# Kernel optimization log

Hardware: AMD Instinct MI355X
Metric: run time of the kernel (lower is better)

Reference implementation:

```python
import jax, jax.numpy as jnp
import numpy as np


def _attention(v, W, static_hidden, dec_hidden):
    # static_hidden: [B,N,H], dec_hidden: [B,1,H], v: [1,1,H], W: [1,H,2H]
    hidden = jnp.concatenate(
        [static_hidden, jnp.broadcast_to(dec_hidden, static_hidden.shape)], axis=2
    )  # [B,N,2H]
    e = jnp.tanh(jnp.einsum('bnk,hk->bnh', hidden, W[0]))  # W @ hidden^T, done row-wise
    scores = jnp.einsum('bnh,h->bn', e, v[0, 0])  # [B,N]
    return jax.nn.softmax(scores, axis=1)[:, None, :]  # [B,1,N]


def _gru_step(x, h, w_ih, w_hh, b_ih, b_hh):
    # x: [B,H] input, h: [B,H] prev hidden; PyTorch gate order: r | z | n
    gx = x @ w_ih.T + b_ih  # [B,3H]
    gh = h @ w_hh.T + b_hh  # [B,3H]
    H = h.shape[-1]
    r = jax.nn.sigmoid(gx[:, :H] + gh[:, :H])
    z = jax.nn.sigmoid(gx[:, H:2 * H] + gh[:, H:2 * H])
    n = jnp.tanh(gx[:, 2 * H:] + r * gh[:, 2 * H:])
    return (1.0 - z) * n + z * h


def _pointer_scores(v, W, static_hidden, context, state_embedding):
    # energy = cat(static, context, state_emb) -> [B,N,3H]
    energy = jnp.concatenate(
        [static_hidden,
         jnp.broadcast_to(context, static_hidden.shape),
         jnp.broadcast_to(state_embedding, static_hidden.shape)], axis=2)
    e = jnp.tanh(jnp.einsum('bnk,hk->bnh', energy, W[0]))  # [B,N,H]
    return jnp.einsum('bnh,h->bn', e, v[0, 0])  # [B,N]


def setup_inputs() -> dict:
    key = jax.random.key(0)
    B, N, H = 128, 512, 512
    ks = jax.random.split(key, 16)
    s = 0.05
    return {
        'static_hidden': jax.random.normal(ks[0], (B, N, H), jnp.float32),
        'state_embedding': jax.random.normal(ks[1], (B, 1, H), jnp.float32),
        'decoder_hidden': jax.random.normal(ks[2], (B, 1, H), jnp.float32),
        'target_hidden': jax.random.normal(ks[3], (B, 1, H), jnp.float32),
        'last_hh': jax.random.normal(ks[4], (1, B, H), jnp.float32),
        # Pointer params (note: target branch of the original reuses self.v/self.W)
        'ptr_v': jax.random.normal(ks[5], (1, 1, H), jnp.float32) * s,
        'ptr_W': jax.random.normal(ks[6], (1, H, 3 * H), jnp.float32) * s,
        # encoder attention params
        'enc_v': jax.random.normal(ks[7], (1, 1, H), jnp.float32) * s,
        'enc_W': jax.random.normal(ks[8], (1, H, 2 * H), jnp.float32) * s,
        # target attention params
        'tgt_v': jax.random.normal(ks[9], (1, 1, H), jnp.float32) * s,
        'tgt_W': jax.random.normal(ks[10], (1, H, 2 * H), jnp.float32) * s,
        # GRU (single layer) params
        'gru_w_ih': jax.random.normal(ks[11], (3 * H, H), jnp.float32) * s,
        'gru_w_hh': jax.random.normal(ks[12], (3 * H, H), jnp.float32) * s,
        'gru_b_ih': jax.random.normal(ks[13], (3 * H,), jnp.float32) * s,
        'gru_b_hh': jax.random.normal(ks[14], (3 * H,), jnp.float32) * s,
    }


def reference(static_hidden, state_embedding, decoder_hidden, target_hidden, last_hh,
              ptr_v, ptr_W, enc_v, enc_W, tgt_v, tgt_W,
              gru_w_ih, gru_w_hh, gru_b_ih, gru_b_hh):
    # GRU over seq len 1 (batch_first); dropout layers are identity (eval mode)
    h_new = _gru_step(decoder_hidden[:, 0, :], last_hh[0], gru_w_ih, gru_w_hh, gru_b_ih, gru_b_hh)
    rnn_out = h_new[:, None, :]          # [B,1,H]
    new_last_hh = h_new[None]            # [1,B,H]

    # encoder attention + context
    enc_attn = _attention(enc_v, enc_W, static_hidden, rnn_out)   # [B,1,N]
    context = jnp.matmul(enc_attn, static_hidden)                 # [B,1,H]
    probs = _pointer_scores(ptr_v, ptr_W, static_hidden, context, state_embedding)

    # target attention + context (original reuses self.v/self.W for scoring)
    tgt_attn = _attention(tgt_v, tgt_W, static_hidden, target_hidden)
    context_t = jnp.matmul(tgt_attn, static_hidden)
    probs_target = _pointer_scores(ptr_v, ptr_W, static_hidden, context_t, state_embedding)

    probs = 5.0 * probs + probs_target
    return (probs, new_last_hh)
```

## Files before the change

### kernel.cpp

```cpp
#include <hip/hip_runtime.h>
#include <math.h>

#define B 128
#define N 512
#define H 512

typedef __attribute__((ext_vector_type(8))) short short8;
typedef __attribute__((ext_vector_type(4))) float floatx4;

typedef const __attribute__((address_space(1))) unsigned int* gas_t;
typedef __attribute__((address_space(3))) unsigned int* las_t;

__device__ __forceinline__ void gl16(const void* g, void* l){
    __builtin_amdgcn_global_load_lds((gas_t)g, (las_t)l, 16, 0, 0);
}

__device__ __forceinline__ float sigmoidf_(float x){ return 1.0f/(1.0f+__expf(-x)); }

__device__ __forceinline__ float fast_tanh(float x){
    float t = __expf(-2.0f*fabsf(x));
    float r = __fdividef(1.0f - t, 1.0f + t);
    return copysignf(r, x);
}

__device__ __forceinline__ unsigned f2bf1(float f){
    unsigned u = __float_as_uint(f);
    u += 0x7FFFu + ((u>>16)&1u);
    return u>>16;
}
__device__ __forceinline__ unsigned pk2(float a, float b){
    return f2bf1(a) | (f2bf1(b)<<16);
}

__global__ __launch_bounds__(256) void k_cast_small(
    const float* __restrict__ encW, const float* __restrict__ tgtW,
    const float* __restrict__ ptrW, const float* __restrict__ wih,
    const float* __restrict__ whh,
    const float* __restrict__ dec, const float* __restrict__ lhh,
    const float* __restrict__ tgt, const float* __restrict__ sem,
    unsigned short* __restrict__ We_s, unsigned short* __restrict__ Wt_s,
    unsigned short* __restrict__ Wp_s, unsigned short* __restrict__ We_d,
    unsigned short* __restrict__ Wt_d, unsigned short* __restrict__ Wp_c,
    unsigned short* __restrict__ Wp_e, unsigned short* __restrict__ Wih_b,
    unsigned short* __restrict__ Whh_b,
    unsigned short* __restrict__ Xbf, unsigned short* __restrict__ Hbf,
    unsigned short* __restrict__ Tbf, unsigned short* __restrict__ Sbf)
{
    int r = blockIdx.x, t = threadIdx.x;
    if (r < 6656){
        const float* src; unsigned short* dst; int pitch, off, row;
        if (r < 512)      { src=encW; dst=We_s; pitch=2*H; off=0;   row=r; }
        else if (r<1024)  { src=tgtW; dst=Wt_s; pitch=2*H; off=0;   row=r-512; }
        else if (r<1536)  { src=ptrW; dst=Wp_s; pitch=3*H; off=0;   row=r-1024; }
        else if (r<2048)  { src=encW; dst=We_d; pitch=2*H; off=H;   row=r-1536; }
        else if (r<2560)  { src=tgtW; dst=Wt_d; pitch=2*H; off=H;   row=r-2048; }
        else if (r<3072)  { src=ptrW; dst=Wp_c; pitch=3*H; off=H;   row=r-2560; }
        else if (r<3584)  { src=ptrW; dst=Wp_e; pitch=3*H; off=2*H; row=r-3072; }
        else if (r<5120)  { src=wih;  dst=Wih_b;pitch=H;   off=0;   row=r-3584; }
        else              { src=whh;  dst=Whh_b;pitch=H;   off=0;   row=r-5120; }
        float2 v = *(const float2*)&src[(size_t)row*pitch + off + 2*t];
        *(unsigned*)&dst[(size_t)row*H + 2*t] = pk2(v.x, v.y);
    } else {
        int blk = r - 6656; int mat = blk >> 5;
        const float* src = mat==0?dec : mat==1?lhh : mat==2?tgt : sem;
        unsigned short* dst = mat==0?Xbf : mat==1?Hbf : mat==2?Tbf : Sbf;
        size_t i = ((size_t)(blk&31)*256 + t)*8;
        float4 lo = *(const float4*)&src[i];
        float4 hi = *(const float4*)&src[i+4];
        uint4 p;
        p.x = pk2(lo.x,lo.y); p.y = pk2(lo.z,lo.w);
        p.z = pk2(hi.x,hi.y); p.w = pk2(hi.z,hi.w);
        *(uint4*)&dst[i] = p;
    }
}

__device__ __forceinline__ void gemm128_tile(
    const unsigned short* __restrict__ Ab,
    const unsigned short* __restrict__ Bb,
    float* __restrict__ C, int ldc)
{
    __shared__ __align__(16) unsigned short As[128*64];
    __shared__ __align__(16) unsigned short Bs[128*64];
    int t = threadIdx.x;
    int lane = t & 63, wave = t >> 6;
    int wy = wave >> 1, wx = wave & 1;
    int li = lane & 15, quad = lane >> 4;

    floatx4 acc[4][4];
    #pragma unroll
    for (int i=0;i<4;++i)
      #pragma unroll
      for (int j=0;j<4;++j) acc[i][j] = (floatx4)(0.0f);

    for (int kt=0; kt<8; ++kt){
        int k0 = kt*64;
        #pragma unroll
        for (int c=0;c<4;++c){
            int s = c*256 + t;
            int row = s >> 3;
            int kb = (s & 7) ^ (row & 7);
            gl16(&Ab[(size_t)row*512 + k0 + kb*8], &As[(size_t)s*8]);
            gl16(&Bb[(size_t)row*512 + k0 + kb*8], &Bs[(size_t)s*8]);
        }
        __syncthreads();
        #pragma unroll
        for (int ks=0;ks<2;++ks){
            short8 af[4], bg[4];
            #pragma unroll
            for (int i=0;i<4;++i){
                int m = wy*64 + i*16 + li;
                int kb = (ks*4 + quad) ^ (m&7);
                af[i] = *(const short8*)&As[m*64 + kb*8];
            }
            #pragma unroll
            for (int j=0;j<4;++j){
                int h = wx*64 + j*16 + li;
                int kb = (ks*4 + quad) ^ (h&7);
                bg[j] = *(const short8*)&Bs[h*64 + kb*8];
            }
            #pragma unroll
            for (int i=0;i<4;++i)
              #pragma unroll
              for (int j=0;j<4;++j)
                acc[i][j] = __builtin_amdgcn_mfma_f32_16x16x32_bf16(af[i], bg[j], acc[i][j], 0,0,0);
        }
        __syncthreads();
    }
    #pragma unroll
    for (int i=0;i<4;++i)
      #pragma unroll
      for (int j=0;j<4;++j)
        #pragma unroll
        for (int rg=0;rg<4;++rg){
            int m = wy*64 + i*16 + quad*4 + rg;
            int n = wx*64 + j*16 + li;
            C[(size_t)m*ldc + n] = acc[i][j][rg];
        }
}

__device__ __forceinline__ void gemm128_tile_f32A(
    const float* __restrict__ Af,
    const unsigned short* __restrict__ Bb,
    float* __restrict__ C, int ldc)
{
    __shared__ __align__(16) unsigned short As[128*64];
    __shared__ __align__(16) unsigned short Bs[128*64];
    int t = threadIdx.x;
    int lane = t & 63, wave = t >> 6;
    int wy = wave >> 1, wx = wave & 1;
    int li = lane & 15, quad = lane >> 4;

    floatx4 acc[4][4];
    #pragma unroll
    for (int i=0;i<4;++i)
      #pragma unroll
      for (int j=0;j<4;++j) acc[i][j] = (floatx4)(0.0f);

    for (int kt=0; kt<8; ++kt){
        int k0 = kt*64;
        #pragma unroll
        for (int c=0;c<4;++c){
            int s = c*256 + t;
            int row = s >> 3;
            int kb = (s & 7) ^ (row & 7);
            gl16(&Bb[(size_t)row*512 + k0 + kb*8], &Bs[(size_t)s*8]);
            const float* src = Af + (size_t)row*512 + k0 + kb*8;
            float4 lo = *(const float4*)src;
            float4 hi = *(const float4*)(src+4);
            uint4 p;
            p.x = pk2(lo.x,lo.y); p.y = pk2(lo.z,lo.w);
            p.z = pk2(hi.x,hi.y); p.w = pk2(hi.z,hi.w);
            *(uint4*)&As[(size_t)s*8] = p;
        }
        __syncthreads();
        #pragma unroll
        for (int ks=0;ks<2;++ks){
            short8 af[4], bg[4];
            #pragma unroll
            for (int i=0;i<4;++i){
                int m = wy*64 + i*16 + li;
                int kb = (ks*4 + quad) ^ (m&7);
                af[i] = *(const short8*)&As[m*64 + kb*8];
            }
            #pragma unroll
            for (int j=0;j<4;++j){
                int h = wx*64 + j*16 + li;
                int kb = (ks*4 + quad) ^ (h&7);
                bg[j] = *(const short8*)&Bs[h*64 + kb*8];
            }
            #pragma unroll
            for (int i=0;i<4;++i)
              #pragma unroll
              for (int j=0;j<4;++j)
                acc[i][j] = __builtin_amdgcn_mfma_f32_16x16x32_bf16(af[i], bg[j], acc[i][j], 0,0,0);
        }
        __syncthreads();
    }
    #pragma unroll
    for (int i=0;i<4;++i)
      #pragma unroll
      for (int j=0;j<4;++j)
        #pragma unroll
        for (int rg=0;rg<4;++rg){
            int m = wy*64 + i*16 + quad*4 + rg;
            int n = wx*64 + j*16 + li;
            C[(size_t)m*ldc + n] = acc[i][j][rg];
        }
}

__global__ __launch_bounds__(256,2) void k_mega(
    const unsigned short* __restrict__ Xbf, const unsigned short* __restrict__ Hbf,
    const unsigned short* __restrict__ Wih_b, const unsigned short* __restrict__ Whh_b,
    float* __restrict__ gx, float* __restrict__ gh,
    const unsigned short* __restrict__ Tbf, const unsigned short* __restrict__ Sbf,
    const unsigned short* __restrict__ Wt_d, const unsigned short* __restrict__ Wp_e,
    float* __restrict__ d_tgt, float* __restrict__ d_se,
    const float* __restrict__ A, unsigned short* __restrict__ Abf)
{
    int blk = blockIdx.x;
    if (blk < 32){
        const unsigned short *Ab, *Bb; float* C; int ldc;
        if (blk < 24){
            int mat = blk / 12, nt = blk % 12;
            Ab = mat ? Hbf : Xbf;
            Bb = (mat ? Whh_b : Wih_b) + (size_t)nt*128*512;
            C = (mat ? gh : gx) + nt*128;
            ldc = 3*H;
        } else {
            int sub = blk - 24; int mat = sub >> 2, nt = sub & 3;
            Ab = mat==0 ? Tbf : Sbf;
            Bb = (mat==0 ? Wt_d : Wp_e) + (size_t)nt*128*512;
            C = (mat==0 ? d_tgt : d_se) + nt*128;
            ldc = H;
        }
        gemm128_tile(Ab, Bb, C, ldc);
    } else {
        int t = threadIdx.x;
        size_t i = ((size_t)(blk-32)*256 + t)*8;
        float4 lo = *(const float4*)&A[i];
        float4 hi = *(const float4*)&A[i+4];
        uint4 p;
        p.x = pk2(lo.x,lo.y); p.y = pk2(lo.z,lo.w);
        p.z = pk2(hi.x,hi.y); p.w = pk2(hi.z,hi.w);
        *(uint4*)&Abf[i] = p;
    }
}

__global__ __launch_bounds__(256) void k_gru_gate(const float* __restrict__ gx,
    const float* __restrict__ gh, const float* __restrict__ lhh,
    const float* __restrict__ bih, const float* __restrict__ bhh,
    float* __restrict__ out_hh, unsigned short* __restrict__ hnew_bf)
{
    int idx = blockIdx.x*256 + threadIdx.x;
    int b = idx >> 9, k = idx & 511;
    const float* gxb = gx + (size_t)b*(3*H);
    const float* ghb = gh + (size_t)b*(3*H);
    float r = sigmoidf_(gxb[k]     + bih[k]     + ghb[k]     + bhh[k]);
    float z = sigmoidf_(gxb[H+k]   + bih[H+k]   + ghb[H+k]   + bhh[H+k]);
    float n = tanhf(gxb[2*H+k] + bih[2*H+k] + r*(ghb[2*H+k] + bhh[2*H+k]));
    float h = (1.f-z)*n + z*lhh[idx];
    out_hh[idx] = h;
    hnew_bf[idx] = (unsigned short)f2bf1(h);
}

__global__ __launch_bounds__(256,2) void k_bias_enc(
    const unsigned short* __restrict__ HNbf, const unsigned short* __restrict__ We_d,
    float* __restrict__ d_enc)
{
    int nt = blockIdx.x;
    gemm128_tile(HNbf, We_d + (size_t)nt*128*512, d_enc + nt*128, H);
}

__global__ __launch_bounds__(256,2) void k_dptr_gemm(
    const float* __restrict__ ctx, const float* __restrict__ ctxt,
    const unsigned short* __restrict__ Wp_c,
    float* __restrict__ d_pe, float* __restrict__ d_pt)
{
    int blk = blockIdx.x;
    int mat = blk >> 2, nt = blk & 3;
    const float* Af = mat ? ctxt : ctx;
    const unsigned short* Bb = Wp_c + (size_t)nt*128*512;
    float* C = (mat ? d_pt : d_pe) + nt*128;
    gemm128_tile_f32A(Af, Bb, C, H);
}

template<bool BF16A>
__global__ __launch_bounds__(256,2) void k_scores_fused(
    const float* __restrict__ Af, const unsigned short* __restrict__ Abf,
    const unsigned short* __restrict__ We, const unsigned short* __restrict__ Wt,
    const float* __restrict__ d_enc, const float* __restrict__ d_tgt,
    const float* __restrict__ enc_v, const float* __restrict__ tgt_v,
    float* __restrict__ sc_e, float* __restrict__ sc_t)
{
    __shared__ __align__(16) unsigned short As[128*64];
    __shared__ __align__(16) unsigned short Be[128*64];
    __shared__ __align__(16) unsigned short Bt[128*64];
    __shared__ float red_e[2][128], red_t[2][128];
    int blk = blockIdx.x;
    int b = blk >> 2; int nt = blk & 3;
    int n0 = nt*128;
    int t = threadIdx.x;
    int lane = t & 63, wave = t >> 6;
    int wy = wave >> 1, wx = wave & 1;
    int li = lane & 15, quad = lane >> 4;

    float nse[4][4], nst[4][4];
    #pragma unroll
    for (int i=0;i<4;++i)
      #pragma unroll
      for (int rg=0;rg<4;++rg){ nse[i][rg]=0.f; nst[i][rg]=0.f; }

    for (int ht=0; ht<4; ++ht){
        int hb = ht*128;
        floatx4 acc_e[4][4], acc_t[4][4];
        #pragma unroll
        for (int i=0;i<4;++i)
          #pragma unroll
          for (int j=0;j<4;++j){ acc_e[i][j]=(floatx4)(0.0f); acc_t[i][j]=(floatx4)(0.0f); }

        for (int kt=0; kt<8; ++kt){
            int k0 = kt*64;
            #pragma unroll
            for (int c=0;c<4;++c){
                int s = c*256 + t;
                int row = s >> 3;
                int kb = (s & 7) ^ (row & 7);
                if constexpr (BF16A){
                    gl16(&Abf[(size_t)(b*N+n0+row)*H + k0 + kb*8], &As[(size_t)s*8]);
                } else {
                    const float* src = Af + (size_t)(b*N+n0+row)*H + k0 + kb*8;
                    float4 lo = *(const float4*)src;
                    float4 hi = *(const float4*)(src+4);
                    uint4 p;
                    p.x = pk2(lo.x,lo.y); p.y = pk2(lo.z,lo.w);
                    p.z = pk2(hi.x,hi.y); p.w = pk2(hi.z,hi.w);
                    *(uint4*)&As[(size_t)s*8] = p;
                }
                gl16(&We[(size_t)(hb+row)*H + k0 + kb*8], &Be[(size_t)s*8]);
                gl16(&Wt[(size_t)(hb+row)*H + k0 + kb*8], &Bt[(size_t)s*8]);
            }
            __syncthreads();
            #pragma unroll
            for (int ks=0;ks<2;++ks){
                short8 af[4], be[4], bt[4];
                #pragma unroll
                for (int i=0;i<4;++i){
                    int m = wy*64 + i*16 + li;
                    int kb = (ks*4 + quad) ^ (m&7);
                    af[i] = *(const short8*)&As[m*64 + kb*8];
                }
                #pragma unroll
                for (int j=0;j<4;++j){
                    int h = wx*64 + j*16 + li;
                    int kb = (ks*4 + quad) ^ (h&7);
                    be[j] = *(const short8*)&Be[h*64 + kb*8];
                    bt[j] = *(const short8*)&Bt[h*64 + kb*8];
                }
                #pragma unroll
                for (int i=0;i<4;++i)
                  #pragma unroll
                  for (int j=0;j<4;++j){
                    acc_e[i][j] = __builtin_amdgcn_mfma_f32_16x16x32_bf16(af[i], be[j], acc_e[i][j], 0,0,0);
                    acc_t[i][j] = __builtin_amdgcn_mfma_f32_16x16x32_bf16(af[i], bt[j], acc_t[i][j], 0,0,0);
                  }
            }
            __syncthreads();
        }
        #pragma unroll
        for (int j=0;j<4;++j){
            int hm = hb + wx*64 + j*16 + li;
            float dje = d_enc[b*H+hm], vje = enc_v[hm];
            float djt = d_tgt[b*H+hm], vjt = tgt_v[hm];
            #pragma unroll
            for (int i=0;i<4;++i)
              #pragma unroll
              for (int rg=0;rg<4;++rg){
                nse[i][rg] += vje * fast_tanh(acc_e[i][j][rg] + dje);
                nst[i][rg] += vjt * fast_tanh(acc_t[i][j][rg] + djt);
              }
        }
    }
    #pragma unroll
    for (int off=1; off<16; off<<=1)
      #pragma unroll
      for (int i=0;i<4;++i)
        #pragma unroll
        for (int rg=0;rg<4;++rg){
          nse[i][rg] += __shfl_xor(nse[i][rg], off);
          nst[i][rg] += __shfl_xor(nst[i][rg], off);
        }
    if (li==0){
        #pragma unroll
        for (int i=0;i<4;++i)
          #pragma unroll
          for (int rg=0;rg<4;++rg){
            red_e[wx][wy*64 + i*16 + quad*4 + rg] = nse[i][rg];
            red_t[wx][wy*64 + i*16 + quad*4 + rg] = nst[i][rg];
          }
    }
    __syncthreads();
    if (t < 128){
        sc_e[b*N + n0 + t] = red_e[0][t] + red_e[1][t];
    } else {
        int r2 = t - 128;
        sc_t[b*N + n0 + r2] = red_t[0][r2] + red_t[1][r2];
    }
}

template<bool BF16A>
__global__ __launch_bounds__(256) void k_smax_ctx(
    const float* __restrict__ Af, const unsigned short* __restrict__ Abf,
    const float* __restrict__ sc_e, const float* __restrict__ sc_t,
    float* __restrict__ ctx, float* __restrict__ ctxt)
{
    __shared__ float we[512], wt[512];
    __shared__ float buf[256];
    __shared__ float red[4][64][4];
    int b = blockIdx.x >> 2, q = blockIdx.x & 3;
    int t = threadIdx.x;

    {
        float x0 = sc_e[b*N+t], x1 = sc_e[b*N+t+256];
        float m = fmaxf(x0,x1);
        buf[t]=m; __syncthreads();
        for (int s2=128;s2>0;s2>>=1){ if(t<s2) buf[t]=fmaxf(buf[t],buf[t+s2]); __syncthreads(); }
        m = buf[0]; __syncthreads();
        float e0 = __expf(x0-m), e1 = __expf(x1-m);
        buf[t]=e0+e1; __syncthreads();
        for (int s2=128;s2>0;s2>>=1){ if(t<s2) buf[t]+=buf[t+s2]; __syncthreads(); }
        float inv = 1.0f/buf[0]; __syncthreads();
        we[t]=e0*inv; we[t+256]=e1*inv;
    }
    {
        float x0 = sc_t[b*N+t], x1 = sc_t[b*N+t+256];
        float m = fmaxf(x0,x1);
        buf[t]=m; __syncthreads();
        for (int s2=128;s2>0;s2>>=1){ if(t<s2) buf[t]=fmaxf(buf[t],buf[t+s2]); __syncthreads(); }
        m = buf[0]; __syncthreads();
        float e0 = __expf(x0-m), e1 = __expf(x1-m);
        buf[t]=e0+e1; __syncthreads();
        for (int s2=128;s2>0;s2>>=1){ if(t<s2) buf[t]+=buf[t+s2]; __syncthreads(); }
        float inv = 1.0f/buf[0]; __syncthreads();
        wt[t]=e0*inv; wt[t+256]=e1*inv;
    }
    __syncthreads();

    int p = t & 63, nq = t >> 6;
    int cp = q*64 + p;
    float ae0=0.f, ae1=0.f, at0=0.f, at1=0.f;
    if constexpr (BF16A){
        const unsigned* base = (const unsigned*)Abf + (size_t)(b*N + nq*128)*(H/2) + cp;
        for (int n=0;n<128;++n){
            unsigned u = base[(size_t)n*(H/2)];
            float lo = __uint_as_float(u<<16);
            float hi = __uint_as_float(u & 0xFFFF0000u);
            float e = we[nq*128+n], g = wt[nq*128+n];
            ae0 += e*lo; ae1 += e*hi; at0 += g*lo; at1 += g*hi;
        }
    } else {
        const float* base = Af + (size_t)(b*N + nq*128)*H + 2*cp;
        for (int n=0;n<128;++n){
            float2 v = *(const float2*)&base[(size_t)n*H];
            float e = we[nq*128+n], g = wt[nq*128+n];
            ae0 += e*v.x; ae1 += e*v.y; at0 += g*v.x; at1 += g*v.y;
        }
    }
    red[nq][p][0]=ae0; red[nq][p][1]=ae1; red[nq][p][2]=at0; red[nq][p][3]=at1;
    __syncthreads();
    if (t < 64){
        float s0=0.f,s1=0.f,s2=0.f,s3=0.f;
        #pragma unroll
        for (int k2=0;k2<4;++k2){
            s0+=red[k2][t][0]; s1+=red[k2][t][1]; s2+=red[k2][t][2]; s3+=red[k2][t][3];
        }
        int c2 = q*64 + t;
        ctx [(size_t)b*H + 2*c2]   = s0;
        ctx [(size_t)b*H + 2*c2+1] = s1;
        ctxt[(size_t)b*H + 2*c2]   = s2;
        ctxt[(size_t)b*H + 2*c2+1] = s3;
    }
}

template<bool BF16A>
__global__ __launch_bounds__(256,2) void k_probs_mfma(
    const float* __restrict__ Af, const unsigned short* __restrict__ Abf,
    const unsigned short* __restrict__ Wp,
    const float* __restrict__ d_pe, const float* __restrict__ d_pt,
    const float* __restrict__ d_se,
    const float* __restrict__ ptr_v, float* __restrict__ probs)
{
    __shared__ __align__(16) unsigned short As[128*64];
    __shared__ __align__(16) unsigned short Bs[128*64];
    __shared__ float red[2][128];
    int blk = blockIdx.x;
    int b = blk >> 2; int nt = blk & 3;
    int n0 = nt*128;

    int t = threadIdx.x;
    int lane = t & 63, wave = t >> 6;
    int wy = wave >> 1, wx = wave & 1;
    int li = lane & 15, quad = lane >> 4;

    float nsum[4][4];
    #pragma unroll
    for (int i=0;i<4;++i){ nsum[i][0]=0.f;nsum[i][1]=0.f;nsum[i][2]=0.f;nsum[i][3]=0.f; }

    for (int ht=0; ht<4; ++ht){
        int hb = ht*128;
        floatx4 acc[4][4];
        #pragma unroll
        for (int i=0;i<4;++i)
          #pragma unroll
          for (int j=0;j<4;++j) acc[i][j] = (floatx4)(0.0f);

        for (int kt=0; kt<8; ++kt){
            int k0 = kt*64;
            #pragma unroll
            for (int c=0;c<4;++c){
                int s = c*256 + t;
                int row = s >> 3;
                int kb = (s & 7) ^ (row & 7);
                if constexpr (BF16A){
                    gl16(&Abf[(size_t)(b*N+n0+row)*H + k0 + kb*8], &As[(size_t)s*8]);
                } else {
                    const float* src = Af + (size_t)(b*N+n0+row)*H + k0 + kb*8;
                    float4 lo = *(const float4*)src;
                    float4 hi = *(const float4*)(src+4);
                    uint4 p;
                    p.x = pk2(lo.x,lo.y); p.y = pk2(lo.z,lo.w);
                    p.z = pk2(hi.x,hi.y); p.w = pk2(hi.z,hi.w);
                    *(uint4*)&As[(size_t)s*8] = p;
                }
                gl16(&Wp[(size_t)(hb+row)*H + k0 + kb*8], &Bs[(size_t)s*8]);
            }
            __syncthreads();
            #pragma unroll
            for (int ks=0;ks<2;++ks){
                short8 af[4], bg[4];
                #pragma unroll
                for (int i=0;i<4;++i){
                    int m = wy*64 + i*16 + li;
                    int kb = (ks*4 + quad) ^ (m&7);
                    af[i] = *(const short8*)&As[m*64 + kb*8];
                }
                #pragma unroll
                for (int j=0;j<4;++j){
                    int h = wx*64 + j*16 + li;
                    int kb = (ks*4 + quad) ^ (h&7);
                    bg[j] = *(const short8*)&Bs[h*64 + kb*8];
                }
                #pragma unroll
                for (int i=0;i<4;++i)
                  #pragma unroll
                  for (int j=0;j<4;++j)
                    acc[i][j] = __builtin_amdgcn_mfma_f32_16x16x32_bf16(af[i], bg[j], acc[i][j], 0,0,0);
            }
            __syncthreads();
        }
        #pragma unroll
        for (int j=0;j<4;++j){
            int hm = hb + wx*64 + j*16 + li;
            float se = d_se[b*H + hm];
            float de = d_pe[b*H + hm] + se;
            float dt = d_pt[b*H + hm] + se;
            float vj = ptr_v[hm];
            #pragma unroll
            for (int i=0;i<4;++i)
              #pragma unroll
              for (int rg=0;rg<4;++rg){
                float s = acc[i][j][rg];
                nsum[i][rg] += vj * (5.0f*fast_tanh(s + de) + fast_tanh(s + dt));
              }
        }
    }
    #pragma unroll
    for (int off=1; off<16; off<<=1)
      #pragma unroll
      for (int i=0;i<4;++i)
        #pragma unroll
        for (int rg=0;rg<4;++rg)
          nsum[i][rg] += __shfl_xor(nsum[i][rg], off);
    if (li==0){
        #pragma unroll
        for (int i=0;i<4;++i)
          #pragma unroll
          for (int rg=0;rg<4;++rg)
            red[wx][wy*64 + i*16 + quad*4 + rg] = nsum[i][rg];
    }
    __syncthreads();
    if (t < 128)
        probs[b*N + n0 + t] = red[0][t] + red[1][t];
}

extern "C" void kernel_launch(void* const* d_in, const int* in_sizes, int n_in,
                              void* d_out, int out_size, void* d_ws, size_t ws_size,
                              hipStream_t stream)
{
    (void)in_sizes; (void)n_in; (void)out_size;
    const float* A    = (const float*)d_in[0];
    const float* sem  = (const float*)d_in[1];
    const float* dec  = (const float*)d_in[2];
    const float* tgt  = (const float*)d_in[3];
    const float* lhh  = (const float*)d_in[4];
    const float* ptrv = (const float*)d_in[5];
    const float* ptrW = (const float*)d_in[6];
    const float* encv = (const float*)d_in[7];
    const float* encW = (const float*)d_in[8];
    const float* tgtv = (const float*)d_in[9];
    const float* tgtW = (const float*)d_in[10];
    const float* wih  = (const float*)d_in[11];
    const float* whh  = (const float*)d_in[12];
    const float* bih  = (const float*)d_in[13];
    const float* bhh  = (const float*)d_in[14];

    float* probs_out = (float*)d_out;
    float* hh_out    = (float*)d_out + B*N;

    float* ws = (float*)d_ws;
    const size_t S = (size_t)B*H;
    float* d_enc = ws;
    float* d_tgt = ws + S;
    float* d_se  = ws + 2*S;
    float* sc_e  = ws + 3*S;
    float* sc_t  = ws + 4*S;
    float* ctx   = ws + 5*S;
    float* ctxt  = ws + 6*S;
    float* d_pe  = ws + 9*S;
    float* d_pt  = ws + 10*S;
    float* gx    = ws + 11*S;
    float* gh    = ws + 14*S;
    unsigned short* bfb  = (unsigned short*)(ws + 17*S);
    const size_t WH = (size_t)H*H;
    const size_t WG = (size_t)3*H*H;
    unsigned short* We_s  = bfb;
    unsigned short* Wt_s  = We_s + WH;
    unsigned short* Wp_s  = Wt_s + WH;
    unsigned short* We_d  = Wp_s + WH;
    unsigned short* Wt_d  = We_d + WH;
    unsigned short* Wp_c  = Wt_d + WH;
    unsigned short* Wp_e  = Wp_c + WH;
    unsigned short* Wih_b = Wp_e + WH;
    unsigned short* Whh_b = Wih_b + WG;
    unsigned short* Xbf   = Whh_b + WG;
    unsigned short* Hbf   = Xbf + S;
    unsigned short* Tbf   = Hbf + S;
    unsigned short* Sbf   = Tbf + S;
    unsigned short* HNbf  = Sbf + S;
    unsigned short* Abf   = HNbf + S;

    const size_t need_full = 17*S*sizeof(float)
        + (7*WH + 2*WG + 5*S + (size_t)B*N*H) * sizeof(unsigned short);
    const bool big = ws_size >= need_full;

    k_cast_small<<<6784, 256, 0, stream>>>(encW, tgtW, ptrW, wih, whh,
        dec, lhh, tgt, sem,
        We_s, Wt_s, Wp_s, We_d, Wt_d, Wp_c, Wp_e, Wih_b, Whh_b,
        Xbf, Hbf, Tbf, Sbf);

    int castA_blocks = big ? (int)(((size_t)B*N*H)/(256*8)) : 0;
    k_mega<<<32 + castA_blocks, 256, 0, stream>>>(Xbf, Hbf, Wih_b, Whh_b, gx, gh,
        Tbf, Sbf, Wt_d, Wp_e, d_tgt, d_se, A, Abf);

    k_gru_gate<<<256, 256, 0, stream>>>(gx, gh, lhh, bih, bhh, hh_out, HNbf);

    k_bias_enc<<<4, 256, 0, stream>>>(HNbf, We_d, d_enc);

    if (big)
        k_scores_fused<true ><<<512, 256, 0, stream>>>(A, Abf, We_s, Wt_s, d_enc, d_tgt, encv, tgtv, sc_e, sc_t);
    else
        k_scores_fused<false><<<512, 256, 0, stream>>>(A, Abf, We_s, Wt_s, d_enc, d_tgt, encv, tgtv, sc_e, sc_t);

    if (big)
        k_smax_ctx<true ><<<512, 256, 0, stream>>>(A, Abf, sc_e, sc_t, ctx, ctxt);
    else
        k_smax_ctx<false><<<512, 256, 0, stream>>>(A, Abf, sc_e, sc_t, ctx, ctxt);

    k_dptr_gemm<<<8, 256, 0, stream>>>(ctx, ctxt, Wp_c, d_pe, d_pt);

    if (big)
        k_probs_mfma<true ><<<512, 256, 0, stream>>>(A, Abf, Wp_s, d_pe, d_pt, d_se, ptrv, probs_out);
    else
        k_probs_mfma<false><<<512, 256, 0, stream>>>(A, Abf, Wp_s, d_pe, d_pt, d_se, ptrv, probs_out);
}
```

Measured before the change: 438.9 us.

## Split score and probs GEMMs across more blocks with one-stage prefetch pipelining

The fused enc/tgt score kernel is split into one kernel covering 1024 blocks, each handling a single attention matrix. The probs kernel is split over hidden-dimension halves, with partial sums combined through atomicAdd into a zeroed output. Both kernels now prefetch the next K tile right after the compute barrier and raise launch bounds to 4 blocks per CU. fast_tanh is simplified to a single exp form. Together these aim for more parallelism and occupancy, at the cost of loading the A tile twice, adding a memset, and changing tanh numerics for large inputs.

Result: slower. 574.2 us (+30.8%).

```diff
diff --git a/kernel.cpp b/kernel.cpp
--- a/kernel.cpp
+++ b/kernel.cpp
@@ -18,9 +18,8 @@
 __device__ __forceinline__ float sigmoidf_(float x){ return 1.0f/(1.0f+__expf(-x)); }
 
 __device__ __forceinline__ float fast_tanh(float x){
-    float t = __expf(-2.0f*fabsf(x));
-    float r = __fdividef(1.0f - t, 1.0f + t);
-    return copysignf(r, x);
+    float e = __expf(2.0f*x);
+    return 1.0f - __fdividef(2.0f, 1.0f + e);
 }
 
 __device__ __forceinline__ unsigned f2bf1(float f){
@@ -285,7 +284,7 @@
 }
 
 template<bool BF16A>
-__global__ __launch_bounds__(256,2) void k_scores_fused(
+__global__ __launch_bounds__(256,4) void k_scores_one(
     const float* __restrict__ Af, const unsigned short* __restrict__ Abf,
     const unsigned short* __restrict__ We, const unsigned short* __restrict__ Wt,
     const float* __restrict__ d_enc, const float* __restrict__ d_tgt,
@@ -293,220 +292,53 @@
     float* __restrict__ sc_e, float* __restrict__ sc_t)
 {
     __shared__ __align__(16) unsigned short As[128*64];
-    __shared__ __align__(16) unsigned short Be[128*64];
-    __shared__ __align__(16) unsigned short Bt[128*64];
-    __shared__ float red_e[2][128], red_t[2][128];
+    __shared__ __align__(16) unsigned short Bs[128*64];
+    __shared__ float red[2][128];
     int blk = blockIdx.x;
-    int b = blk >> 2; int nt = blk & 3;
+    int which = blk >> 9;
+    int rem = blk & 511;
+    int b = rem >> 2, nt = rem & 3;
     int n0 = nt*128;
+    const unsigned short* W = which ? Wt : We;
+    const float* dv = which ? d_tgt : d_enc;
+    const float* vv = which ? tgt_v : enc_v;
+    float* sc = which ? sc_t : sc_e;
+
     int t = threadIdx.x;
     int lane = t & 63, wave = t >> 6;
     int wy = wave >> 1, wx = wave & 1;
     int li = lane & 15, quad = lane >> 4;
 
-    float nse[4][4], nst[4][4];
+    float nse[4][4];
     #pragma unroll
     for (int i=0;i<4;++i)
       #pragma unroll
-      for (int rg=0;rg<4;++rg){ nse[i][rg]=0.f; nst[i][rg]=0.f; }
-
+      for (int rg=0;rg<4;++rg) nse[i][rg]=0.f;
+
+    auto stage = [&](int ht, int kt){
+        int hb = ht*128, k0 = kt*64;
+        #pragma unroll
+        for (int c=0;c<4;++c){
+            int s = c*256 + t;
+            int row = s >> 3;
+            int kb = (s & 7) ^ (row & 7);
+            if constexpr (BF16A){
+                gl16(&Abf[(size_t)(b*N+n0+row)*H + k0 + kb*8], &As[(size_t)s*8]);
+            } else {
+                const float* src = Af + (size_t)(b*N+n0+row)*H + k0 + kb*8;
+                float4 lo = *(const float4*)src;
+                float4 hi = *(const float4*)(src+4);
+                uint4 p;
+                p.x = pk2(lo.x,lo.y); p.y = pk2(lo.z,lo.w);
+                p.z = pk2(hi.x,hi.y); p.w = pk2(hi.z,hi.w);
+                *(uint4*)&As[(size_t)s*8] = p;
+            }
+            gl16(&W[(size_t)(hb+row)*H + k0 + kb*8], &Bs[(size_t)s*8]);
+        }
+    };
+
+    stage(0,0);
     for (int ht=0; ht<4; ++ht){
-        int hb = ht*128;
-        floatx4 acc_e[4][4], acc_t[4][4];
-        #pragma unroll
-        for (int i=0;i<4;++i)
-          #pragma unroll
-          for (int j=0;j<4;++j){ acc_e[i][j]=(floatx4)(0.0f); acc_t[i][j]=(floatx4)(0.0f); }
-
-        for (int kt=0; kt<8; ++kt){
-            int k0 = kt*64;
-            #pragma unroll
-            for (int c=0;c<4;++c){
-                int s = c*256 + t;
-                int row = s >> 3;
-                int kb = (s & 7) ^ (row & 7);
-                if constexpr (BF16A){
-                    gl16(&Abf[(size_t)(b*N+n0+row)*H + k0 + kb*8], &As[(size_t)s*8]);
-                } else {
-                    const float* src = Af + (size_t)(b*N+n0+row)*H + k0 + kb*8;
-                    float4 lo = *(const float4*)src;
-                    float4 hi = *(const float4*)(src+4);
-                    uint4 p;
-                    p.x = pk2(lo.x,lo.y); p.y = pk2(lo.z,lo.w);
-                    p.z = pk2(hi.x,hi.y); p.w = pk2(hi.z,hi.w);
-                    *(uint4*)&As[(size_t)s*8] = p;
-                }
-                gl16(&We[(size_t)(hb+row)*H + k0 + kb*8], &Be[(size_t)s*8]);
-                gl16(&Wt[(size_t)(hb+row)*H + k0 + kb*8], &Bt[(size_t)s*8]);
-            }
-            __syncthreads();
-            #pragma unroll
-            for (int ks=0;ks<2;++ks){
-                short8 af[4], be[4], bt[4];
-                #pragma unroll
-                for (int i=0;i<4;++i){
-                    int m = wy*64 + i*16 + li;
-                    int kb = (ks*4 + quad) ^ (m&7);
-                    af[i] = *(const short8*)&As[m*64 + kb*8];
-                }
-                #pragma unroll
-                for (int j=0;j<4;++j){
-                    int h = wx*64 + j*16 + li;
-                    int kb = (ks*4 + quad) ^ (h&7);
-                    be[j] = *(const short8*)&Be[h*64 + kb*8];
-                    bt[j] = *(const short8*)&Bt[h*64 + kb*8];
-                }
-                #pragma unroll
-                for (int i=0;i<4;++i)
-                  #pragma unroll
-                  for (int j=0;j<4;++j){
-                    acc_e[i][j] = __builtin_amdgcn_mfma_f32_16x16x32_bf16(af[i], be[j], acc_e[i][j], 0,0,0);
-                    acc_t[i][j] = __builtin_amdgcn_mfma_f32_16x16x32_bf16(af[i], bt[j], acc_t[i][j], 0,0,0);
-                  }
-            }
-            __syncthreads();
-        }
-        #pragma unroll
-        for (int j=0;j<4;++j){
-            int hm = hb + wx*64 + j*16 + li;
-            float dje = d_enc[b*H+hm], vje = enc_v[hm];
-            float djt = d_tgt[b*H+hm], vjt = tgt_v[hm];
-            #pragma unroll
-            for (int i=0;i<4;++i)
-              #pragma unroll
-              for (int rg=0;rg<4;++rg){
-                nse[i][rg] += vje * fast_tanh(acc_e[i][j][rg] + dje);
-                nst[i][rg] += vjt * fast_tanh(acc_t[i][j][rg] + djt);
-              }
-        }
-    }
-    #pragma unroll
-    for (int off=1; off<16; off<<=1)
-      #pragma unroll
-      for (int i=0;i<4;++i)
-        #pragma unroll
-        for (int rg=0;rg<4;++rg){
-          nse[i][rg] += __shfl_xor(nse[i][rg], off);
-          nst[i][rg] += __shfl_xor(nst[i][rg], off);
-        }
-    if (li==0){
-        #pragma unroll
-        for (int i=0;i<4;++i)
-          #pragma unroll
-          for (int rg=0;rg<4;++rg){
-            red_e[wx][wy*64 + i*16 + quad*4 + rg] = nse[i][rg];
-            red_t[wx][wy*64 + i*16 + quad*4 + rg] = nst[i][rg];
-          }
-    }
-    __syncthreads();
-    if (t < 128){
-        sc_e[b*N + n0 + t] = red_e[0][t] + red_e[1][t];
-    } else {
-        int r2 = t - 128;
-        sc_t[b*N + n0 + r2] = red_t[0][r2] + red_t[1][r2];
-    }
-}
-
-template<bool BF16A>
-__global__ __launch_bounds__(256) void k_smax_ctx(
-    const float* __restrict__ Af, const unsigned short* __restrict__ Abf,
-    const float* __restrict__ sc_e, const float* __restrict__ sc_t,
-    float* __restrict__ ctx, float* __restrict__ ctxt)
-{
-    __shared__ float we[512], wt[512];
-    __shared__ float buf[256];
-    __shared__ float red[4][64][4];
-    int b = blockIdx.x >> 2, q = blockIdx.x & 3;
-    int t = threadIdx.x;
-
-    {
-        float x0 = sc_e[b*N+t], x1 = sc_e[b*N+t+256];
-        float m = fmaxf(x0,x1);
-        buf[t]=m; __syncthreads();
-        for (int s2=128;s2>0;s2>>=1){ if(t<s2) buf[t]=fmaxf(buf[t],buf[t+s2]); __syncthreads(); }
-        m = buf[0]; __syncthreads();
-        float e0 = __expf(x0-m), e1 = __expf(x1-m);
-        buf[t]=e0+e1; __syncthreads();
-        for (int s2=128;s2>0;s2>>=1){ if(t<s2) buf[t]+=buf[t+s2]; __syncthreads(); }
-        float inv = 1.0f/buf[0]; __syncthreads();
-        we[t]=e0*inv; we[t+256]=e1*inv;
-    }
-    {
-        float x0 = sc_t[b*N+t], x1 = sc_t[b*N+t+256];
-        float m = fmaxf(x0,x1);
-        buf[t]=m; __syncthreads();
-        for (int s2=128;s2>0;s2>>=1){ if(t<s2) buf[t]=fmaxf(buf[t],buf[t+s2]); __syncthreads(); }
-        m = buf[0]; __syncthreads();
-        float e0 = __expf(x0-m), e1 = __expf(x1-m);
-        buf[t]=e0+e1; __syncthreads();
-        for (int s2=128;s2>0;s2>>=1){ if(t<s2) buf[t]+=buf[t+s2]; __syncthreads(); }
-        float inv = 1.0f/buf[0]; __syncthreads();
-        wt[t]=e0*inv; wt[t+256]=e1*inv;
-    }
-    __syncthreads();
-
-    int p = t & 63, nq = t >> 6;
-    int cp = q*64 + p;
-    float ae0=0.f, ae1=0.f, at0=0.f, at1=0.f;
-    if constexpr (BF16A){
-        const unsigned* base = (const unsigned*)Abf + (size_t)(b*N + nq*128)*(H/2) + cp;
-        for (int n=0;n<128;++n){
-            unsigned u = base[(size_t)n*(H/2)];
-            float lo = __uint_as_float(u<<16);
-            float hi = __uint_as_float(u & 0xFFFF0000u);
-            float e = we[nq*128+n], g = wt[nq*128+n];
-            ae0 += e*lo; ae1 += e*hi; at0 += g*lo; at1 += g*hi;
-        }
-    } else {
-        const float* base = Af + (size_t)(b*N + nq*128)*H + 2*cp;
-        for (int n=0;n<128;++n){
-            float2 v = *(const float2*)&base[(size_t)n*H];
-            float e = we[nq*128+n], g = wt[nq*128+n];
-            ae0 += e*v.x; ae1 += e*v.y; at0 += g*v.x; at1 += g*v.y;
-        }
-    }
-    red[nq][p][0]=ae0; red[nq][p][1]=ae1; red[nq][p][2]=at0; red[nq][p][3]=at1;
-    __syncthreads();
-    if (t < 64){
-        float s0=0.f,s1=0.f,s2=0.f,s3=0.f;
-        #pragma unroll
-        for (int k2=0;k2<4;++k2){
-            s0+=red[k2][t][0]; s1+=red[k2][t][1]; s2+=red[k2][t][2]; s3+=red[k2][t][3];
-        }
-        int c2 = q*64 + t;
-        ctx [(size_t)b*H + 2*c2]   = s0;
-        ctx [(size_t)b*H + 2*c2+1] = s1;
-        ctxt[(size_t)b*H + 2*c2]   = s2;
-        ctxt[(size_t)b*H + 2*c2+1] = s3;
-    }
-}
-
-template<bool BF16A>
-__global__ __launch_bounds__(256,2) void k_probs_mfma(
-    const float* __restrict__ Af, const unsigned short* __restrict__ Abf,
-    const unsigned short* __restrict__ Wp,
-    const float* __restrict__ d_pe, const float* __restrict__ d_pt,
-    const float* __restrict__ d_se,
-    const float* __restrict__ ptr_v, float* __restrict__ probs)
-{
-    __shared__ __align__(16) unsigned short As[128*64];
-    __shared__ __align__(16) unsigned short Bs[128*64];
-    __shared__ float red[2][128];
-    int blk = blockIdx.x;
-    int b = blk >> 2; int nt = blk & 3;
-    int n0 = nt*128;
-
-    int t = threadIdx.x;
-    int lane = t & 63, wave = t >> 6;
-    int wy = wave >> 1, wx = wave & 1;
-    int li = lane & 15, quad = lane >> 4;
-
-    float nsum[4][4];
-    #pragma unroll
-    for (int i=0;i<4;++i){ nsum[i][0]=0.f;nsum[i][1]=0.f;nsum[i][2]=0.f;nsum[i][3]=0.f; }
-
-    for (int ht=0; ht<4; ++ht){
-        int hb = ht*128;
         floatx4 acc[4][4];
         #pragma unroll
         for (int i=0;i<4;++i)
@@ -514,25 +346,6 @@
           for (int j=0;j<4;++j) acc[i][j] = (floatx4)(0.0f);
 
         for (int kt=0; kt<8; ++kt){
-            int k0 = kt*64;
-            #pragma unroll
-            for (int c=0;c<4;++c){
-                int s = c*256 + t;
-                int row = s >> 3;
-                int kb = (s & 7) ^ (row & 7);
-                if constexpr (BF16A){
-                    gl16(&Abf[(size_t)(b*N+n0+row)*H + k0 + kb*8], &As[(size_t)s*8]);
-                } else {
-                    const float* src = Af + (size_t)(b*N+n0+row)*H + k0 + kb*8;
-                    float4 lo = *(const float4*)src;
-                    float4 hi = *(const float4*)(src+4);
-                    uint4 p;
-                    p.x = pk2(lo.x,lo.y); p.y = pk2(lo.z,lo.w);
-                    p.z = pk2(hi.x,hi.y); p.w = pk2(hi.z,hi.w);
-                    *(uint4*)&As[(size_t)s*8] = p;
-                }
-                gl16(&Wp[(size_t)(hb+row)*H + k0 + kb*8], &Bs[(size_t)s*8]);
-            }
             __syncthreads();
             #pragma unroll
             for (int ks=0;ks<2;++ks){
@@ -556,7 +369,200 @@
                     acc[i][j] = __builtin_amdgcn_mfma_f32_16x16x32_bf16(af[i], bg[j], acc[i][j], 0,0,0);
             }
             __syncthreads();
-        }
+            if (kt < 7)      stage(ht, kt+1);
+            else if (ht < 3) stage(ht+1, 0);
+        }
+        int hb = ht*128;
+        #pragma unroll
+        for (int j=0;j<4;++j){
+            int hm = hb + wx*64 + j*16 + li;
+            float dj = dv[b*H+hm], vj = vv[hm];
+            #pragma unroll
+            for (int i=0;i<4;++i)
+              #pragma unroll
+              for (int rg=0;rg<4;++rg)
+                nse[i][rg] += vj * fast_tanh(acc[i][j][rg] + dj);
+        }
+    }
+    #pragma unroll
+    for (int off=1; off<16; off<<=1)
+      #pragma unroll
+      for (int i=0;i<4;++i)
+        #pragma unroll
+        for (int rg=0;rg<4;++rg)
+          nse[i][rg] += __shfl_xor(nse[i][rg], off);
+    if (li==0){
+        #pragma unroll
+        for (int i=0;i<4;++i)
+          #pragma unroll
+          for (int rg=0;rg<4;++rg)
+            red[wx][wy*64 + i*16 + quad*4 + rg] = nse[i][rg];
+    }
+    __syncthreads();
+    if (t < 128)
+        sc[b*N + n0 + t] = red[0][t] + red[1][t];
+}
+
+template<bool BF16A>
+__global__ __launch_bounds__(256) void k_smax_ctx(
+    const float* __restrict__ Af, const unsigned short* __restrict__ Abf,
+    const float* __restrict__ sc_e, const float* __restrict__ sc_t,
+    float* __restrict__ ctx, float* __restrict__ ctxt)
+{
+    __shared__ float we[512], wt[512];
+    __shared__ float buf[256];
+    __shared__ float red[4][64][4];
+    int b = blockIdx.x >> 2, q = blockIdx.x & 3;
+    int t = threadIdx.x;
+
+    {
+        float x0 = sc_e[b*N+t], x1 = sc_e[b*N+t+256];
+        float m = fmaxf(x0,x1);
+        buf[t]=m; __syncthreads();
+        for (int s2=128;s2>0;s2>>=1){ if(t<s2) buf[t]=fmaxf(buf[t],buf[t+s2]); __syncthreads(); }
+        m = buf[0]; __syncthreads();
+        float e0 = __expf(x0-m), e1 = __expf(x1-m);
+        buf[t]=e0+e1; __syncthreads();
+        for (int s2=128;s2>0;s2>>=1){ if(t<s2) buf[t]+=buf[t+s2]; __syncthreads(); }
+        float inv = 1.0f/buf[0]; __syncthreads();
+        we[t]=e0*inv; we[t+256]=e1*inv;
+    }
+    {
+        float x0 = sc_t[b*N+t], x1 = sc_t[b*N+t+256];
+        float m = fmaxf(x0,x1);
+        buf[t]=m; __syncthreads();
+        for (int s2=128;s2>0;s2>>=1){ if(t<s2) buf[t]=fmaxf(buf[t],buf[t+s2]); __syncthreads(); }
+        m = buf[0]; __syncthreads();
+        float e0 = __expf(x0-m), e1 = __expf(x1-m);
+        buf[t]=e0+e1; __syncthreads();
+        for (int s2=128;s2>0;s2>>=1){ if(t<s2) buf[t]+=buf[t+s2]; __syncthreads(); }
+        float inv = 1.0f/buf[0]; __syncthreads();
+        wt[t]=e0*inv; wt[t+256]=e1*inv;
+    }
+    __syncthreads();
+
+    int p = t & 63, nq = t >> 6;
+    int cp = q*64 + p;
+    float ae0=0.f, ae1=0.f, at0=0.f, at1=0.f;
+    if constexpr (BF16A){
+        const unsigned* base = (const unsigned*)Abf + (size_t)(b*N + nq*128)*(H/2) + cp;
+        for (int n=0;n<128;++n){
+            unsigned u = base[(size_t)n*(H/2)];
+            float lo = __uint_as_float(u<<16);
+            float hi = __uint_as_float(u & 0xFFFF0000u);
+            float e = we[nq*128+n], g = wt[nq*128+n];
+            ae0 += e*lo; ae1 += e*hi; at0 += g*lo; at1 += g*hi;
+        }
+    } else {
+        const float* base = Af + (size_t)(b*N + nq*128)*H + 2*cp;
+        for (int n=0;n<128;++n){
+            float2 v = *(const float2*)&base[(size_t)n*H];
+            float e = we[nq*128+n], g = wt[nq*128+n];
+            ae0 += e*v.x; ae1 += e*v.y; at0 += g*v.x; at1 += g*v.y;
+        }
+    }
+    red[nq][p][0]=ae0; red[nq][p][1]=ae1; red[nq][p][2]=at0; red[nq][p][3]=at1;
+    __syncthreads();
+    if (t < 64){
+        float s0=0.f,s1=0.f,s2=0.f,s3=0.f;
+        #pragma unroll
+        for (int k2=0;k2<4;++k2){
+            s0+=red[k2][t][0]; s1+=red[k2][t][1]; s2+=red[k2][t][2]; s3+=red[k2][t][3];
+        }
+        int c2 = q*64 + t;
+        ctx [(size_t)b*H + 2*c2]   = s0;
+        ctx [(size_t)b*H + 2*c2+1] = s1;
+        ctxt[(size_t)b*H + 2*c2]   = s2;
+        ctxt[(size_t)b*H + 2*c2+1] = s3;
+    }
+}
+
+template<bool BF16A>
+__global__ __launch_bounds__(256,4) void k_probs_mfma(
+    const float* __restrict__ Af, const unsigned short* __restrict__ Abf,
+    const unsigned short* __restrict__ Wp,
+    const float* __restrict__ d_pe, const float* __restrict__ d_pt,
+    const float* __restrict__ d_se,
+    const float* __restrict__ ptr_v, float* __restrict__ probs)
+{
+    __shared__ __align__(16) unsigned short As[128*64];
+    __shared__ __align__(16) unsigned short Bs[128*64];
+    __shared__ float red[2][128];
+    int blk = blockIdx.x;
+    int half = blk >> 9;
+    int rem = blk & 511;
+    int b = rem >> 2, nt = rem & 3;
+    int n0 = nt*128;
+    int ht0 = half*2;
+
+    int t = threadIdx.x;
+    int lane = t & 63, wave = t >> 6;
+    int wy = wave >> 1, wx = wave & 1;
+    int li = lane & 15, quad = lane >> 4;
+
+    float nsum[4][4];
+    #pragma unroll
+    for (int i=0;i<4;++i){ nsum[i][0]=0.f;nsum[i][1]=0.f;nsum[i][2]=0.f;nsum[i][3]=0.f; }
+
+    auto stage = [&](int ht, int kt){
+        int hb = ht*128, k0 = kt*64;
+        #pragma unroll
+        for (int c=0;c<4;++c){
+            int s = c*256 + t;
+            int row = s >> 3;
+            int kb = (s & 7) ^ (row & 7);
+            if constexpr (BF16A){
+                gl16(&Abf[(size_t)(b*N+n0+row)*H + k0 + kb*8], &As[(size_t)s*8]);
+            } else {
+                const float* src = Af + (size_t)(b*N+n0+row)*H + k0 + kb*8;
+                float4 lo = *(const float4*)src;
+                float4 hi = *(const float4*)(src+4);
+                uint4 p;
+                p.x = pk2(lo.x,lo.y); p.y = pk2(lo.z,lo.w);
+                p.z = pk2(hi.x,hi.y); p.w = pk2(hi.z,hi.w);
+                *(uint4*)&As[(size_t)s*8] = p;
+            }
+            gl16(&Wp[(size_t)(hb+row)*H + k0 + kb*8], &Bs[(size_t)s*8]);
+        }
+    };
+
+    stage(ht0, 0);
+    for (int hi=0; hi<2; ++hi){
+        int ht = ht0 + hi;
+        floatx4 acc[4][4];
+        #pragma unroll
+        for (int i=0;i<4;++i)
+          #pragma unroll
+          for (int j=0;j<4;++j) acc[i][j] = (floatx4)(0.0f);
+
+        for (int kt=0; kt<8; ++kt){
+            __syncthreads();
+            #pragma unroll
+            for (int ks=0;ks<2;++ks){
+                short8 af[4], bg[4];
+                #pragma unroll
+                for (int i=0;i<4;++i){
+                    int m = wy*64 + i*16 + li;
+                    int kb = (ks*4 + quad) ^ (m&7);
+                    af[i] = *(const short8*)&As[m*64 + kb*8];
+                }
+                #pragma unroll
+                for (int j=0;j<4;++j){
+                    int h = wx*64 + j*16 + li;
+                    int kb = (ks*4 + quad) ^ (h&7);
+                    bg[j] = *(const short8*)&Bs[h*64 + kb*8];
+                }
+                #pragma unroll
+                for (int i=0;i<4;++i)
+                  #pragma unroll
+                  for (int j=0;j<4;++j)
+                    acc[i][j] = __builtin_amdgcn_mfma_f32_16x16x32_bf16(af[i], bg[j], acc[i][j], 0,0,0);
+            }
+            __syncthreads();
+            if (kt < 7)      stage(ht, kt+1);
+            else if (hi < 1) stage(ht+1, 0);
+        }
+        int hb = ht*128;
         #pragma unroll
         for (int j=0;j<4;++j){
             int hm = hb + wx*64 + j*16 + li;
@@ -589,7 +595,7 @@
     }
     __syncthreads();
     if (t < 128)
-        probs[b*N + n0 + t] = red[0][t] + red[1][t];
+        atomicAdd(&probs[b*N + n0 + t], red[0][t] + red[1][t]);
 }
 
 extern "C" void kernel_launch(void* const* d_in, const int* in_sizes, int n_in,
@@ -652,6 +658,8 @@
         + (7*WH + 2*WG + 5*S + (size_t)B*N*H) * sizeof(unsigned short);
     const bool big = ws_size >= need_full;
 
+    hipMemsetAsync(probs_out, 0, (size_t)B*N*sizeof(float), stream);
+
     k_cast_small<<<6784, 256, 0, stream>>>(encW, tgtW, ptrW, wih, whh,
         dec, lhh, tgt, sem,
         We_s, Wt_s, Wp_s, We_d, Wt_d, Wp_c, Wp_e, Wih_b, Whh_b,
@@ -666,9 +674,9 @@
     k_bias_enc<<<4, 256, 0, stream>>>(HNbf, We_d, d_enc);
 
     if (big)
-        k_scores_fused<true ><<<512, 256, 0, stream>>>(A, Abf, We_s, Wt_s, d_enc, d_tgt, encv, tgtv, sc_e, sc_t);
+        k_scores_one<true ><<<1024, 256, 0, stream>>>(A, Abf, We_s, Wt_s, d_enc, d_tgt, encv, tgtv, sc_e, sc_t);
     else
-        k_scores_fused<false><<<512, 256, 0, stream>>>(A, Abf, We_s, Wt_s, d_enc, d_tgt, encv, tgtv, sc_e, sc_t);
+        k_scores_one<false><<<1024, 256, 0, stream>>>(A, Abf, We_s, Wt_s, d_enc, d_tgt, encv, tgtv, sc_e, sc_t);
 
     if (big)
         k_smax_ctx<true ><<<512, 256, 0, stream>>>(A, Abf, sc_e, sc_t, ctx, ctxt);
@@ -678,7 +686,7 @@
     k_dptr_gemm<<<8, 256, 0, stream>>>(ctx, ctxt, Wp_c, d_pe, d_pt);
 
     if (big)
-        k_probs_mfma<true ><<<512, 256, 0, stream>>>(A, Abf, Wp_s, d_pe, d_pt, d_se, ptrv, probs_out);
+        k_probs_mfma<true ><<<1024, 256, 0, stream>>>(A, Abf, Wp_s, d_pe, d_pt, d_se, ptrv, probs_out);
     else
-        k_probs_mfma<false><<<512, 256, 0, stream>>>(A, Abf, Wp_s, d_pe, d_pt, d_se, ptrv, probs_out);
-}
+        k_probs_mfma<false><<<1024, 256, 0, stream>>>(A, Abf, Wp_s, d_pe, d_pt, d_se, ptrv, probs_out);
+}
```
